# Kernel tuning notes

Measured on AMD Instinct MI355X. Metric: run time of the kernel, lower is better.

## Reference

```python
import jax, jax.numpy as jnp
import numpy as np

BSZ, SEQ, DIM, NH = 2, 2048, 2048, 16
HD = DIM // NH  # 128


def setup_inputs() -> dict:
    key = jax.random.key(0)
    ks = jax.random.split(key, 6)
    x = jax.random.normal(ks[0], (BSZ, SEQ, DIM), dtype=jnp.float32)
    # torch Linear weights: [out_features, in_features]
    scale = 1.0 / np.sqrt(DIM)
    wq = jax.random.normal(ks[1], (DIM, DIM), dtype=jnp.float32) * scale
    wk = jax.random.normal(ks[2], (DIM, DIM), dtype=jnp.float32) * scale
    wv = jax.random.normal(ks[3], (DIM, DIM), dtype=jnp.float32) * scale
    wo = jax.random.normal(ks[4], (DIM, DIM), dtype=jnp.float32) * scale
    # RoPE freqs (llama style): theta=10000
    inv_freq = 1.0 / (10000.0 ** (jnp.arange(0, HD, 2, dtype=jnp.float32) / HD))  # [HD//2]
    t = jnp.arange(SEQ, dtype=jnp.float32)
    angles = jnp.outer(t, inv_freq)  # [SEQ, HD//2]
    freqs_cos = jnp.cos(angles)
    freqs_sin = jnp.sin(angles)
    # causal additive mask [SEQ, SEQ]
    mask = jnp.where(jnp.tril(jnp.ones((SEQ, SEQ), dtype=bool)), 0.0, -jnp.inf).astype(jnp.float32)
    return {"x": x, "wq": wq, "wk": wk, "wv": wv, "wo": wo,
            "freqs_cos": freqs_cos, "freqs_sin": freqs_sin, "mask": mask}


def _apply_rope(v, cos, sin):
    # v: [b, s, h, hd]; complex pairs are interleaved (even=real, odd=imag)
    b, s, h, hd = v.shape
    vr = v.reshape(b, s, h, hd // 2, 2)
    v0, v1 = vr[..., 0], vr[..., 1]
    c = cos[None, :, None, :]  # [1, s, 1, hd//2]
    sn = sin[None, :, None, :]
    out = jnp.stack([v0 * c - v1 * sn, v0 * sn + v1 * c], axis=-1)
    return out.reshape(b, s, h, hd)


def reference(x, wq, wk, wv, wo, freqs_cos, freqs_sin, mask):
    b, s, _ = x.shape
    xq = (x @ wq.T).reshape(b, s, NH, HD)
    xk = (x @ wk.T).reshape(b, s, NH, HD)
    xv = (x @ wv.T).reshape(b, s, NH, HD)
    xq = _apply_rope(xq, freqs_cos, freqs_sin)
    xk = _apply_rope(xk, freqs_cos, freqs_sin)
    # [b, h, s, s]
    scores = jnp.einsum('bqhd,bkhd->bhqk', xq, xk) / jnp.sqrt(jnp.float32(HD))
    scores = scores + mask[None, None, :, :]
    probs = jax.nn.softmax(scores.astype(jnp.float32), axis=-1).astype(scores.dtype)
    out = jnp.einsum('bhqk,bkhd->bqhd', probs, xv).reshape(b, s, NH * HD)
    return out @ wo.T
```

## Files before the change

### kernel.cpp

```cpp
#include <hip/hip_runtime.h>
#include <hip/hip_bf16.h>
#include <stdint.h>

typedef __bf16 bf16x8 __attribute__((ext_vector_type(8)));
typedef float f32x4 __attribute__((ext_vector_type(4)));
typedef unsigned short u16;
typedef unsigned int u32;

#define DEVI __device__ __forceinline__

DEVI u16 f2b(float f){ __bf16 h = (__bf16)f; return __builtin_bit_cast(u16, h); }
DEVI float b2f(u16 u){ return (float)__builtin_bit_cast(__bf16, u); }

constexpr int BSZ = 2, SEQ = 2048, DIM = 2048, NH = 16, HD = 128;

#if defined(__has_builtin)
#if __has_builtin(__builtin_amdgcn_global_load_lds)
#define HAVE_ASYNC_LDS 1
#endif
#endif

DEVI void cp16(void* lds, const void* g){
#ifdef HAVE_ASYNC_LDS
  auto gp = (const __attribute__((address_space(1))) u32*)(uintptr_t)g;
  auto lp = (__attribute__((address_space(3))) u32*)(uintptr_t)lds;
  __builtin_amdgcn_global_load_lds(gp, lp, 16, 0, 0);
#else
  *(uint4*)lds = *(const uint4*)g;
#endif
}

__global__ __launch_bounds__(256) void k_convert(
    const float* __restrict__ x, const float* __restrict__ wq,
    const float* __restrict__ wk, const float* __restrict__ wv,
    const float* __restrict__ wo,
    u16* __restrict__ xb, u16* __restrict__ wqkv, u16* __restrict__ wob)
{
  int e = (blockIdx.x * 256 + threadIdx.x) * 4;
  float4 v; u16* dp;
  if (e < 8388608){
    v = *(const float4*)&x[e]; dp = &xb[e];
  } else if (e < 20971520){
    int o = e - 8388608; int sec = o >> 22; int oo = o & 4194303;
    const float* w = (sec == 0) ? wq : ((sec == 1) ? wk : wv);
    v = *(const float4*)&w[oo]; dp = &wqkv[o];
  } else {
    int o = e - 20971520;
    v = *(const float4*)&wo[o]; dp = &wob[o];
  }
  ushort4 r; r.x = f2b(v.x); r.y = f2b(v.y); r.z = f2b(v.z); r.w = f2b(v.w);
  *(ushort4*)dp = r;
}

DEVI void gemm_core_256x128(u16* smem, const u16* __restrict__ A, const u16* __restrict__ B,
                            int tm, int tn, int t, f32x4 (&acc)[4][4])
{
  const int lane = t & 63, l15 = lane & 15, quad = lane >> 4;
  const int wave = t >> 6, wm = wave >> 1, wn = wave & 1;
  const int swr = (l15 & 7) << 3;
  const int rb = t >> 3;
  const int csw = ((t & 7) ^ (rb & 7)) << 3;
  const u16* As0 = A + (size_t)(tm + rb) * DIM + csw;
  const u16* Bs0 = B + (size_t)(tn + rb) * DIM + csw;

  auto STAGE = [&](int kt){
    const int buf = kt & 1;
    const int kb = kt * 64;
    u16* d = &smem[buf * 24576 + t * 8];
    #pragma unroll
    for (int p = 0; p < 4; ++p)
      cp16(d + p * 4096, As0 + (size_t)p * (64 * DIM) + kb);
    #pragma unroll
    for (int p = 0; p < 2; ++p)
      cp16(d + 16384 + p * 4096, Bs0 + (size_t)p * (64 * DIM) + kb);
  };

  STAGE(0);
  #pragma unroll 2
  for (int kt = 0; kt < DIM / 64; ++kt){
    __syncthreads();
    if (kt < DIM / 64 - 1) STAGE(kt + 1);
    const u16* Ab = &smem[(kt & 1) * 24576];
    const u16* Bb = Ab + 16384;
    bf16x8 Af[4][2], Bf[4][2];
    #pragma unroll
    for (int mt = 0; mt < 4; ++mt)
      #pragma unroll
      for (int ks = 0; ks < 2; ++ks)
        Af[mt][ks] = *(const bf16x8*)&Ab[(wm * 64 + mt * 16 + l15) * 64 + ((ks * 32 + quad * 8) ^ swr)];
    #pragma unroll
    for (int nt = 0; nt < 4; ++nt)
      #pragma unroll
      for (int ks = 0; ks < 2; ++ks)
        Bf[nt][ks] = *(const bf16x8*)&Bb[(wn * 64 + nt * 16 + l15) * 64 + ((ks * 32 + quad * 8) ^ swr)];
    #pragma unroll
    for (int c = 0; c < 4; ++c){
      const int mb = (c >> 1) * 2, nb = (c & 1) * 2;
      __builtin_amdgcn_s_setprio(1);
      #pragma unroll
      for (int mi = 0; mi < 2; ++mi)
        #pragma unroll
        for (int ni = 0; ni < 2; ++ni)
          #pragma unroll
          for (int ks = 0; ks < 2; ++ks)
            acc[mb + mi][nb + ni] = __builtin_amdgcn_mfma_f32_16x16x32_bf16(
                Af[mb + mi][ks], Bf[nb + ni][ks], acc[mb + mi][nb + ni], 0, 0, 0);
      __builtin_amdgcn_s_setprio(0);
    }
  }
  __syncthreads();
}

__global__ __launch_bounds__(512, 2) void k_gemm_qkv(
    const u16* __restrict__ A, const u16* __restrict__ W,
    const float* __restrict__ fc, const float* __restrict__ fs,
    u16* __restrict__ Qd, u16* __restrict__ Kd, u16* __restrict__ Vd)
{
  __shared__ __align__(16) u16 smem[49152];
  const int t = threadIdx.x;
  const int wg = blockIdx.x;
  const int id = (wg & 7) * 96 + (wg >> 3);
  const int tm = (id & 15) << 8;
  const int tn = (id >> 4) << 7;
  f32x4 acc[4][4] = {};
  gemm_core_256x128(smem, A, W, tm, tn, t, acc);

  const int lane = t & 63, l15 = lane & 15, quad = lane >> 4;
  const int wave = t >> 6, wm = wave >> 1, wn = wave & 1;
  u16* Cs = smem;
  #pragma unroll
  for (int mt = 0; mt < 4; ++mt)
    #pragma unroll
    for (int nt = 0; nt < 4; ++nt)
      #pragma unroll
      for (int r = 0; r < 4; ++r){
        int rin = wm * 64 + mt * 16 + quad * 4 + r;
        int col = wn * 64 + nt * 16 + l15;
        Cs[rin * 128 + ((col + rin * 8) & 127)] = f2b(acc[mt][nt][r]);
      }
  __syncthreads();

  const int sec = tn >> 11;
  const int hh = (tn & 2047) >> 7;
  u16* dst = (sec == 0) ? Qd : ((sec == 1) ? Kd : Vd);
  const float qs = (sec == 0) ? (0.08838834764831845f * 1.4426950408889634f) : 1.0f;
  const int col0 = (t & 15) * 8;
  #pragma unroll
  for (int jj = 0; jj < 8; ++jj){
    int row = (t >> 4) + jj * 32;
    int m = tm + row;
    int b = m >> 11, s = m & 2047;
    uint4 cv = *(const uint4*)&Cs[row * 128 + ((col0 + row * 8) & 127)];
    const u16* cp = (const u16*)&cv;
    u16 op[8];
    if (sec < 2){
      float4 c4 = *(const float4*)&fc[(size_t)s * 64 + (col0 >> 1)];
      float4 s4 = *(const float4*)&fs[(size_t)s * 64 + (col0 >> 1)];
      float cc[4] = {c4.x*qs, c4.y*qs, c4.z*qs, c4.w*qs};
      float ss[4] = {s4.x*qs, s4.y*qs, s4.z*qs, s4.w*qs};
      #pragma unroll
      for (int p = 0; p < 4; ++p){
        float a = b2f(cp[2*p]), bb = b2f(cp[2*p+1]);
        op[2*p]   = f2b(a*cc[p] - bb*ss[p]);
        op[2*p+1] = f2b(a*ss[p] + bb*cc[p]);
      }
    } else {
      #pragma unroll
      for (int p = 0; p < 8; ++p) op[p] = cp[p];
    }
    *(uint4*)&dst[((size_t)(b*NH + hh)*SEQ + s)*HD + col0] = *(const uint4*)op;
  }
}

__global__ __launch_bounds__(256) void k_vtrans(
    const u16* __restrict__ V, u16* __restrict__ Vt)
{
  __shared__ u16 ts[64*72];
  const int t = threadIdx.x;
  const int st = blockIdx.x, dt = blockIdx.y, bh = blockIdx.z;
  const size_t base  = (size_t)bh * SEQ * HD;
  const size_t baseT = (size_t)bh * HD * SEQ;
  #pragma unroll
  for (int i = 0; i < 2; ++i){
    int s = i*32 + (t>>3), c = t&7;
    *(uint4*)&ts[s*72 + c*8] = *(const uint4*)&V[base + (size_t)(st*64 + s)*HD + dt*64 + c*8];
  }
  __syncthreads();
  #pragma unroll
  for (int i = 0; i < 2; ++i){
    int d = i*32 + (t>>3), sc = t&7;
    u16 tmp[8];
    #pragma unroll
    for (int j = 0; j < 8; ++j) tmp[j] = ts[(sc*8 + j)*72 + d];
    *(uint4*)&Vt[baseT + (size_t)(dt*64 + d)*SEQ + st*64 + sc*8] = *(const uint4*)tmp;
  }
}

__global__ __launch_bounds__(512) void k_flash(
    const u16* __restrict__ Qd, const u16* __restrict__ Kd,
    const u16* __restrict__ Vt, u16* __restrict__ OP0, u16* __restrict__ OP1,
    float* __restrict__ Mp, float* __restrict__ Lp)
{
  __shared__ __align__(16) u16 lds[24576];
  const int t = threadIdx.x, lane = t & 63, wave = t >> 6;
  const int l15 = lane & 15, quad = lane >> 4;
  const int swz = (l15 & 7) << 3;

  const int flat = blockIdx.x;
  const int xcd = flat & 7, idx = flat >> 3;
  const int bh = xcd * 4 + (idx >> 4);
  const int x = idx & 15;
  const int b = bh >> 4, h = bh & 15;
  const int j = x >> 1, split = x & 1;

  const size_t base  = (size_t)bh * SEQ * HD;
  const size_t baseT = (size_t)bh * HD * SEQ;
  u16* Ks = lds;
  u16* Vs = lds + 8192;
  u16* Psw = lds + 16384 + wave * 1024;
  u16* OPs = split ? OP1 : OP0;
  const int lo = 17*split, hi = lo + 17;
  const int qt0 = j, qt1 = 15 - j;
  const int len0 = 2*qt0 + 2;

  const int krow = t >> 4, kslot = t & 15;
  const int vrow = t >> 3, vslot = t & 7;

  for (int pass = 0; pass < 2; ++pass){
    const int qt = pass ? qt1 : qt0;
    const int len = 2*qt + 2;
    int kt0 = pass ? (lo - len0) : lo; if (kt0 < 0) kt0 = 0;
    int kt1 = pass ? (hi - len0) : hi; if (kt1 > len) kt1 = len;
    const int qb = qt*128 + wave*16;

    bf16x8 qf[4];
    #pragma unroll
    for (int ks = 0; ks < 4; ++ks)
      qf[ks] = *(const bf16x8*)&Qd[base + (size_t)(qb + l15)*HD + ks*32 + quad*8];

    f32x4 oacc[8] = {};
    float m_s = -1e30f, l_s = 0.f;

    if (kt0 < kt1){
      uint4 kreg[2], vreg[2];
      #pragma unroll
      for (int i = 0; i < 2; ++i){
        kreg[i] = *(const uint4*)&Kd[base + (size_t)(kt0*64 + i*32 + krow)*HD + kslot*8];
        vreg[i] = *(const uint4*)&Vt[baseT + (size_t)(i*64 + vrow)*SEQ + kt0*64 + vslot*8];
      }
      for (int kt = kt0; kt < kt1; ++kt){
        __syncthreads();
        #pragma unroll
        for (int i = 0; i < 2; ++i){
          int kr = i*32 + krow;
          *(uint4*)&Ks[kr*128 + ((kslot*8) ^ ((kr & 7) << 3))] = kreg[i];
          int vr = i*64 + vrow;
          *(uint4*)&Vs[vr*64 + ((vslot ^ (vr & 7)) << 3)] = vreg[i];
        }
        __syncthreads();
        if (kt + 1 < kt1){
          #pragma unroll
          for (int i = 0; i < 2; ++i){
            kreg[i] = *(const uint4*)&Kd[base + (size_t)((kt+1)*64 + i*32 + krow)*HD + kslot*8];
            vreg[i] = *(const uint4*)&Vt[baseT + (size_t)(i*64 + vrow)*SEQ + (kt+1)*64 + vslot*8];
          }
        }
        if (kt*64 <= qb + 15){
          f32x4 sacc[4] = {};
          #pragma unroll
          for (int ks = 0; ks < 4; ++ks){
            bf16x8 kf[4];
            #pragma unroll
            for (int nk = 0; nk < 4; ++nk)
              kf[nk] = *(const bf16x8*)&Ks[(nk*16 + l15)*128 + ((ks*32 + quad*8) ^ swz)];
            __builtin_amdgcn_s_setprio(1);
            #pragma unroll
            for (int nk = 0; nk < 4; ++nk)
              sacc[nk] = __builtin_amdgcn_mfma_f32_16x16x32_bf16(kf[nk], qf[ks], sacc[nk], 0, 0, 0);
            __builtin_amdgcn_s_setprio(0);
          }
          if (kt*64 + 63 > qb){
            int q = qb + l15;
            #pragma unroll
            for (int nk = 0; nk < 4; ++nk)
              #pragma unroll
              for (int r = 0; r < 4; ++r){
                int key = kt*64 + nk*16 + quad*4 + r;
                if (key > q) sacc[nk][r] = -1e30f;
              }
          }
          float m4[4];
          #pragma unroll
          for (int nk = 0; nk < 4; ++nk)
            m4[nk] = fmaxf(fmaxf(sacc[nk][0], sacc[nk][1]), fmaxf(sacc[nk][2], sacc[nk][3]));
          float rm = fmaxf(fmaxf(m4[0], m4[1]), fmaxf(m4[2], m4[3]));
          rm = fmaxf(rm, __shfl_xor(rm, 16));
          rm = fmaxf(rm, __shfl_xor(rm, 32));
          float mnew = fmaxf(m_s, rm);
          float alpha = exp2f(m_s - mnew);
          m_s = mnew;
          float s4[4];
          #pragma unroll
          for (int nk = 0; nk < 4; ++nk){
            u16 pk[4];
            float p0 = exp2f(sacc[nk][0] - mnew);
            float p1 = exp2f(sacc[nk][1] - mnew);
            float p2 = exp2f(sacc[nk][2] - mnew);
            float p3 = exp2f(sacc[nk][3] - mnew);
            pk[0] = f2b(p0); pk[1] = f2b(p1); pk[2] = f2b(p2); pk[3] = f2b(p3);
            s4[nk] = (p0 + p1) + (p2 + p3);
            *(uint2*)&Psw[l15*64 + ((nk*16 + quad*4) ^ swz)] = *(const uint2*)pk;
          }
          float rs = (s4[0] + s4[1]) + (s4[2] + s4[3]);
          rs += __shfl_xor(rs, 16);
          rs += __shfl_xor(rs, 32);
          l_s = l_s*alpha + rs;
          #pragma unroll
          for (int db = 0; db < 8; ++db)
            #pragma unroll
            for (int r = 0; r < 4; ++r) oacc[db][r] *= alpha;
          #pragma unroll
          for (int k2 = 0; k2 < 2; ++k2){
            bf16x8 pf = *(const bf16x8*)&Psw[l15*64 + ((k2*32 + quad*8) ^ swz)];
            __builtin_amdgcn_s_setprio(1);
            #pragma unroll
            for (int db = 0; db < 8; ++db){
              bf16x8 vf = *(const bf16x8*)&Vs[(db*16 + l15)*64 + ((k2*32 + quad*8) ^ swz)];
              oacc[db] = __builtin_amdgcn_mfma_f32_16x16x32_bf16(vf, pf, oacc[db], 0, 0, 0);
            }
            __builtin_amdgcn_s_setprio(0);
          }
        }
      }
    }
    __syncthreads();
    {
      u16* Osw = lds + wave*2048;
      #pragma unroll
      for (int db = 0; db < 8; ++db){
        u16 ok[4];
        #pragma unroll
        for (int r = 0; r < 4; ++r) ok[r] = f2b(oacc[db][r]);
        *(uint2*)&Osw[l15*128 + ((db*16 + quad*4) ^ swz)] = *(const uint2*)ok;
      }
      #pragma unroll
      for (int i = 0; i < 4; ++i){
        int q = i*4 + quad;
        uint4 v = *(const uint4*)&Osw[q*128 + ((l15*8) ^ ((q & 7) << 3))];
        *(uint4*)&OPs[(((size_t)(b*SEQ + qb + q))*NH + h)*HD + l15*8] = v;
      }
      if (quad == 0){
        size_t mi = ((size_t)split*BSZ*NH + bh)*SEQ + (qb + l15);
        Mp[mi] = m_s;
        Lp[mi] = l_s;
      }
    }
  }
}

__global__ __launch_bounds__(256) void k_combine(
    u16* __restrict__ OP0, const u16* __restrict__ OP1,
    const float* __restrict__ Mp, const float* __restrict__ Lp)
{
  size_t flat = ((size_t)blockIdx.x*256 + threadIdx.x)*8;
  int h = (int)((flat >> 7) & 15);
  int s = (int)((flat >> 11) & 2047);
  int b = (int)(flat >> 22);
  size_t row = ((size_t)(b*NH + h))*SEQ + s;
  const size_t off1 = (size_t)BSZ*NH*SEQ;
  float m0 = Mp[row], l0 = Lp[row];
  float m1 = Mp[row + off1], l1 = Lp[row + off1];
  float m = fmaxf(m0, m1);
  float w0 = exp2f(m0 - m), w1 = exp2f(m1 - m);
  float inv = 1.0f / (w0*l0 + w1*l1);
  uint4 a = *(const uint4*)&OP0[flat];
  uint4 c = *(const uint4*)&OP1[flat];
  const u16* pa = (const u16*)&a;
  const u16* pc = (const u16*)&c;
  u16 o[8];
  #pragma unroll
  for (int i = 0; i < 8; ++i)
    o[i] = f2b((b2f(pa[i])*w0 + b2f(pc[i])*w1) * inv);
  *(uint4*)&OP0[flat] = *(const uint4*)o;
}

__global__ __launch_bounds__(512, 2) void k_gemm_out(
    const u16* __restrict__ A, const u16* __restrict__ W, float* __restrict__ out)
{
  __shared__ __align__(16) u16 smem[49152];
  const int t = threadIdx.x;
  const int wg = blockIdx.x;
  const int id = (wg & 7) * 32 + (wg >> 3);
  const int tm = (id & 15) << 8;
  const int tn = (id >> 4) << 7;
  f32x4 acc[4][4] = {};
  gemm_core_256x128(smem, A, W, tm, tn, t, acc);
  const int lane = t & 63, l15 = lane & 15, quad = lane >> 4;
  const int wave = t >> 6, wm = wave >> 1, wn = wave & 1;
  #pragma unroll
  for (int mt = 0; mt < 4; ++mt)
    #pragma unroll
    for (int nt = 0; nt < 4; ++nt)
      #pragma unroll
      for (int r = 0; r < 4; ++r){
        int row = tm + wm*64 + mt*16 + quad*4 + r;
        int col = tn + wn*64 + nt*16 + l15;
        out[(size_t)row*DIM + col] = acc[mt][nt][r];
      }
}

extern "C" void kernel_launch(void* const* d_in, const int* in_sizes, int n_in,
                              void* d_out, int out_size, void* d_ws, size_t ws_size,
                              hipStream_t stream)
{
  const float* x  = (const float*)d_in[0];
  const float* wq = (const float*)d_in[1];
  const float* wk = (const float*)d_in[2];
  const float* wv = (const float*)d_in[3];
  const float* wo = (const float*)d_in[4];
  const float* fc = (const float*)d_in[5];
  const float* fs = (const float*)d_in[6];
  float* out = (float*)d_out;

  char* ws = (char*)d_ws;
  u16* xb   = (u16*)(ws);
  u16* wqkv = (u16*)(ws + 16777216);
  u16* wob  = (u16*)(ws + 41943040);
  u16* Qr   = (u16*)(ws + 50331648);
  u16* Kr   = (u16*)(ws + 67108864);
  u16* Vr   = (u16*)(ws + 83886080);
  u16* Ob   = (u16*)(ws + 100663296);
  u16* VtT  = xb;
  u16* OP1  = wqkv;
  float* Mp = (float*)(ws + 33554432);
  float* Lp = (float*)(ws + 34078720);

  k_convert <<<24576, 256, 0, stream>>>(x, wq, wk, wv, wo, xb, wqkv, wob);
  k_gemm_qkv<<<768, 512, 0, stream>>>(xb, wqkv, fc, fs, Qr, Kr, Vr);
  k_vtrans  <<<dim3(32, 2, 32), 256, 0, stream>>>(Vr, VtT);
  k_flash   <<<512, 512, 0, stream>>>(Qr, Kr, VtT, Ob, OP1, Mp, Lp);
  k_combine <<<4096, 256, 0, stream>>>(Ob, OP1, Mp, Lp);
  k_gemm_out<<<256, 512, 0, stream>>>(Ob, wob, out);
}
```

Baseline: 453.0 us.

## Load K/V fragments directly from global memory per wave, dropping LDS staging and barriers

Each wave now reads its K and V^T MFMA fragments straight from global memory instead of staging shared 64-key tiles in LDS behind block-wide barriers. Each wave also stops its key loop at its own causal limit, so waves no longer idle through tiles that other waves need. This removes the syncthreads and LDS store traffic but multiplies global/L2 reads by the number of waves and exposes load latency with no prefetch. The LDS layout is shrunk to only the P and O staging buffers.

```diff
diff --git a/kernel.cpp b/kernel.cpp
--- a/kernel.cpp
+++ b/kernel.cpp
@@ -215,16 +215,12 @@
 
   const size_t base  = (size_t)bh * SEQ * HD;
   const size_t baseT = (size_t)bh * HD * SEQ;
-  u16* Ks = lds;
-  u16* Vs = lds + 8192;
-  u16* Psw = lds + 16384 + wave * 1024;
+  u16* Psw = lds + wave * 1024;
+  u16* Osw = lds + 8192 + wave * 2048;
   u16* OPs = split ? OP1 : OP0;
   const int lo = 17*split, hi = lo + 17;
   const int qt0 = j, qt1 = 15 - j;
   const int len0 = 2*qt0 + 2;
-
-  const int krow = t >> 4, kslot = t & 15;
-  const int vrow = t >> 3, vslot = t & 7;
 
   for (int pass = 0; pass < 2; ++pass){
     const int qt = pass ? qt1 : qt0;
@@ -232,6 +228,7 @@
     int kt0 = pass ? (lo - len0) : lo; if (kt0 < 0) kt0 = 0;
     int kt1 = pass ? (hi - len0) : hi; if (kt1 > len) kt1 = len;
     const int qb = qt*128 + wave*16;
+    const int ktw = min(kt1, ((qb + 15) >> 6) + 1);
 
     bf16x8 qf[4];
     #pragma unroll
@@ -241,101 +238,75 @@
     f32x4 oacc[8] = {};
     float m_s = -1e30f, l_s = 0.f;
 
-    if (kt0 < kt1){
-      uint4 kreg[2], vreg[2];
-      #pragma unroll
-      for (int i = 0; i < 2; ++i){
-        kreg[i] = *(const uint4*)&Kd[base + (size_t)(kt0*64 + i*32 + krow)*HD + kslot*8];
-        vreg[i] = *(const uint4*)&Vt[baseT + (size_t)(i*64 + vrow)*SEQ + kt0*64 + vslot*8];
-      }
-      for (int kt = kt0; kt < kt1; ++kt){
-        __syncthreads();
-        #pragma unroll
-        for (int i = 0; i < 2; ++i){
-          int kr = i*32 + krow;
-          *(uint4*)&Ks[kr*128 + ((kslot*8) ^ ((kr & 7) << 3))] = kreg[i];
-          int vr = i*64 + vrow;
-          *(uint4*)&Vs[vr*64 + ((vslot ^ (vr & 7)) << 3)] = vreg[i];
-        }
-        __syncthreads();
-        if (kt + 1 < kt1){
+    for (int kt = kt0; kt < ktw; ++kt){
+      f32x4 sacc[4] = {};
+      #pragma unroll
+      for (int ks = 0; ks < 4; ++ks){
+        bf16x8 kf[4];
+        #pragma unroll
+        for (int nk = 0; nk < 4; ++nk)
+          kf[nk] = *(const bf16x8*)&Kd[base + (size_t)(kt*64 + nk*16 + l15)*HD + ks*32 + quad*8];
+        __builtin_amdgcn_s_setprio(1);
+        #pragma unroll
+        for (int nk = 0; nk < 4; ++nk)
+          sacc[nk] = __builtin_amdgcn_mfma_f32_16x16x32_bf16(kf[nk], qf[ks], sacc[nk], 0, 0, 0);
+        __builtin_amdgcn_s_setprio(0);
+      }
+      if (kt*64 + 63 > qb){
+        int q = qb + l15;
+        #pragma unroll
+        for (int nk = 0; nk < 4; ++nk)
           #pragma unroll
-          for (int i = 0; i < 2; ++i){
-            kreg[i] = *(const uint4*)&Kd[base + (size_t)((kt+1)*64 + i*32 + krow)*HD + kslot*8];
-            vreg[i] = *(const uint4*)&Vt[baseT + (size_t)(i*64 + vrow)*SEQ + (kt+1)*64 + vslot*8];
+          for (int r = 0; r < 4; ++r){
+            int key = kt*64 + nk*16 + quad*4 + r;
+            if (key > q) sacc[nk][r] = -1e30f;
           }
-        }
-        if (kt*64 <= qb + 15){
-          f32x4 sacc[4] = {};
-          #pragma unroll
-          for (int ks = 0; ks < 4; ++ks){
-            bf16x8 kf[4];
-            #pragma unroll
-            for (int nk = 0; nk < 4; ++nk)
-              kf[nk] = *(const bf16x8*)&Ks[(nk*16 + l15)*128 + ((ks*32 + quad*8) ^ swz)];
-            __builtin_amdgcn_s_setprio(1);
-            #pragma unroll
-            for (int nk = 0; nk < 4; ++nk)
-              sacc[nk] = __builtin_amdgcn_mfma_f32_16x16x32_bf16(kf[nk], qf[ks], sacc[nk], 0, 0, 0);
-            __builtin_amdgcn_s_setprio(0);
-          }
-          if (kt*64 + 63 > qb){
-            int q = qb + l15;
-            #pragma unroll
-            for (int nk = 0; nk < 4; ++nk)
-              #pragma unroll
-              for (int r = 0; r < 4; ++r){
-                int key = kt*64 + nk*16 + quad*4 + r;
-                if (key > q) sacc[nk][r] = -1e30f;
-              }
-          }
-          float m4[4];
-          #pragma unroll
-          for (int nk = 0; nk < 4; ++nk)
-            m4[nk] = fmaxf(fmaxf(sacc[nk][0], sacc[nk][1]), fmaxf(sacc[nk][2], sacc[nk][3]));
-          float rm = fmaxf(fmaxf(m4[0], m4[1]), fmaxf(m4[2], m4[3]));
-          rm = fmaxf(rm, __shfl_xor(rm, 16));
-          rm = fmaxf(rm, __shfl_xor(rm, 32));
-          float mnew = fmaxf(m_s, rm);
-          float alpha = exp2f(m_s - mnew);
-          m_s = mnew;
-          float s4[4];
-          #pragma unroll
-          for (int nk = 0; nk < 4; ++nk){
-            u16 pk[4];
-            float p0 = exp2f(sacc[nk][0] - mnew);
-            float p1 = exp2f(sacc[nk][1] - mnew);
-            float p2 = exp2f(sacc[nk][2] - mnew);
-            float p3 = exp2f(sacc[nk][3] - mnew);
-            pk[0] = f2b(p0); pk[1] = f2b(p1); pk[2] = f2b(p2); pk[3] = f2b(p3);
-            s4[nk] = (p0 + p1) + (p2 + p3);
-            *(uint2*)&Psw[l15*64 + ((nk*16 + quad*4) ^ swz)] = *(const uint2*)pk;
-          }
-          float rs = (s4[0] + s4[1]) + (s4[2] + s4[3]);
-          rs += __shfl_xor(rs, 16);
-          rs += __shfl_xor(rs, 32);
-          l_s = l_s*alpha + rs;
-          #pragma unroll
-          for (int db = 0; db < 8; ++db)
-            #pragma unroll
-            for (int r = 0; r < 4; ++r) oacc[db][r] *= alpha;
-          #pragma unroll
-          for (int k2 = 0; k2 < 2; ++k2){
-            bf16x8 pf = *(const bf16x8*)&Psw[l15*64 + ((k2*32 + quad*8) ^ swz)];
-            __builtin_amdgcn_s_setprio(1);
-            #pragma unroll
-            for (int db = 0; db < 8; ++db){
-              bf16x8 vf = *(const bf16x8*)&Vs[(db*16 + l15)*64 + ((k2*32 + quad*8) ^ swz)];
-              oacc[db] = __builtin_amdgcn_mfma_f32_16x16x32_bf16(vf, pf, oacc[db], 0, 0, 0);
-            }
-            __builtin_amdgcn_s_setprio(0);
-          }
-        }
+      }
+      float m4[4];
+      #pragma unroll
+      for (int nk = 0; nk < 4; ++nk)
+        m4[nk] = fmaxf(fmaxf(sacc[nk][0], sacc[nk][1]), fmaxf(sacc[nk][2], sacc[nk][3]));
+      float rm = fmaxf(fmaxf(m4[0], m4[1]), fmaxf(m4[2], m4[3]));
+      rm = fmaxf(rm, __shfl_xor(rm, 16));
+      rm = fmaxf(rm, __shfl_xor(rm, 32));
+      float mnew = fmaxf(m_s, rm);
+      float alpha = exp2f(m_s - mnew);
+      m_s = mnew;
+      float s4[4];
+      #pragma unroll
+      for (int nk = 0; nk < 4; ++nk){
+        u16 pk[4];
+        float p0 = exp2f(sacc[nk][0] - mnew);
+        float p1 = exp2f(sacc[nk][1] - mnew);
+        float p2 = exp2f(sacc[nk][2] - mnew);
+        float p3 = exp2f(sacc[nk][3] - mnew);
+        pk[0] = f2b(p0); pk[1] = f2b(p1); pk[2] = f2b(p2); pk[3] = f2b(p3);
+        s4[nk] = (p0 + p1) + (p2 + p3);
+        *(uint2*)&Psw[l15*64 + ((nk*16 + quad*4) ^ swz)] = *(const uint2*)pk;
+      }
+      float rs = (s4[0] + s4[1]) + (s4[2] + s4[3]);
+      rs += __shfl_xor(rs, 16);
+      rs += __shfl_xor(rs, 32);
+      l_s = l_s*alpha + rs;
+      #pragma unroll
+      for (int db = 0; db < 8; ++db)
+        #pragma unroll
+        for (int r = 0; r < 4; ++r) oacc[db][r] *= alpha;
+      #pragma unroll
+      for (int k2 = 0; k2 < 2; ++k2){
+        bf16x8 pf = *(const bf16x8*)&Psw[l15*64 + ((k2*32 + quad*8) ^ swz)];
+        bf16x8 vf[8];
+        #pragma unroll
+        for (int db = 0; db < 8; ++db)
+          vf[db] = *(const bf16x8*)&Vt[baseT + (size_t)(db*16 + l15)*SEQ + kt*64 + k2*32 + quad*8];
+        __builtin_amdgcn_s_setprio(1);
+        #pragma unroll
+        for (int db = 0; db < 8; ++db)
+          oacc[db] = __builtin_amdgcn_mfma_f32_16x16x32_bf16(vf[db], pf, oacc[db], 0, 0, 0);
+        __builtin_amdgcn_s_setprio(0);
       }
     }
-    __syncthreads();
     {
-      u16* Osw = lds + wave*2048;
       #pragma unroll
       for (int db = 0; db < 8; ++db){
         u16 ok[4];
```

After: 546.1 us. 1.21x slower.

## Double-buffer K/V tiles in LDS to halve barriers per key tile

Applied to the files above, without the earlier changes.

Allocates two LDS buffers for the K and V tiles so the next tile is written to the alternate buffer after computing on the current one, needing one barrier per iteration instead of two. The output epilogue now stages through each wave's private P scratch region in two 64-column chunks, so the barrier before the epilogue is dropped. LDS use grows from 48KB to 80KB per block, which may reduce occupancy for the 512-thread blocks.

```diff
diff --git a/kernel.cpp b/kernel.cpp
--- a/kernel.cpp
+++ b/kernel.cpp
@@ -201,7 +201,7 @@
     const u16* __restrict__ Vt, u16* __restrict__ OP0, u16* __restrict__ OP1,
     float* __restrict__ Mp, float* __restrict__ Lp)
 {
-  __shared__ __align__(16) u16 lds[24576];
+  __shared__ __align__(16) u16 lds[40960];
   const int t = threadIdx.x, lane = t & 63, wave = t >> 6;
   const int l15 = lane & 15, quad = lane >> 4;
   const int swz = (l15 & 7) << 3;
@@ -215,9 +215,7 @@
 
   const size_t base  = (size_t)bh * SEQ * HD;
   const size_t baseT = (size_t)bh * HD * SEQ;
-  u16* Ks = lds;
-  u16* Vs = lds + 8192;
-  u16* Psw = lds + 16384 + wave * 1024;
+  u16* Psw = lds + 32768 + wave * 1024;
   u16* OPs = split ? OP1 : OP0;
   const int lo = 17*split, hi = lo + 17;
   const int qt0 = j, qt1 = 15 - j;
@@ -243,36 +241,40 @@
 
     if (kt0 < kt1){
       uint4 kreg[2], vreg[2];
-      #pragma unroll
-      for (int i = 0; i < 2; ++i){
-        kreg[i] = *(const uint4*)&Kd[base + (size_t)(kt0*64 + i*32 + krow)*HD + kslot*8];
-        vreg[i] = *(const uint4*)&Vt[baseT + (size_t)(i*64 + vrow)*SEQ + kt0*64 + vslot*8];
-      }
-      for (int kt = kt0; kt < kt1; ++kt){
-        __syncthreads();
+      auto LOADT = [&](int kt){
+        #pragma unroll
+        for (int i = 0; i < 2; ++i){
+          kreg[i] = *(const uint4*)&Kd[base + (size_t)(kt*64 + i*32 + krow)*HD + kslot*8];
+          vreg[i] = *(const uint4*)&Vt[baseT + (size_t)(i*64 + vrow)*SEQ + kt*64 + vslot*8];
+        }
+      };
+      auto WRITET = [&](int bu){
+        u16* Kb = lds + bu*8192;
+        u16* Vb = lds + 16384 + bu*8192;
         #pragma unroll
         for (int i = 0; i < 2; ++i){
           int kr = i*32 + krow;
-          *(uint4*)&Ks[kr*128 + ((kslot*8) ^ ((kr & 7) << 3))] = kreg[i];
+          *(uint4*)&Kb[kr*128 + ((kslot*8) ^ ((kr & 7) << 3))] = kreg[i];
           int vr = i*64 + vrow;
-          *(uint4*)&Vs[vr*64 + ((vslot ^ (vr & 7)) << 3)] = vreg[i];
-        }
-        __syncthreads();
-        if (kt + 1 < kt1){
-          #pragma unroll
-          for (int i = 0; i < 2; ++i){
-            kreg[i] = *(const uint4*)&Kd[base + (size_t)((kt+1)*64 + i*32 + krow)*HD + kslot*8];
-            vreg[i] = *(const uint4*)&Vt[baseT + (size_t)(i*64 + vrow)*SEQ + (kt+1)*64 + vslot*8];
-          }
-        }
+          *(uint4*)&Vb[vr*64 + ((vslot*8) ^ ((vr & 7) << 3))] = vreg[i];
+        }
+      };
+      LOADT(kt0);
+      WRITET(0);
+      if (kt0 + 1 < kt1) LOADT(kt0 + 1);
+      __syncthreads();
+      int buf = 0;
+      for (int kt = kt0; kt < kt1; ++kt){
         if (kt*64 <= qb + 15){
+          const u16* Kb = lds + buf*8192;
+          const u16* Vb = lds + 16384 + buf*8192;
           f32x4 sacc[4] = {};
           #pragma unroll
           for (int ks = 0; ks < 4; ++ks){
             bf16x8 kf[4];
             #pragma unroll
             for (int nk = 0; nk < 4; ++nk)
-              kf[nk] = *(const bf16x8*)&Ks[(nk*16 + l15)*128 + ((ks*32 + quad*8) ^ swz)];
+              kf[nk] = *(const bf16x8*)&Kb[(nk*16 + l15)*128 + ((ks*32 + quad*8) ^ swz)];
             __builtin_amdgcn_s_setprio(1);
             #pragma unroll
             for (int nk = 0; nk < 4; ++nk)
@@ -325,29 +327,39 @@
             __builtin_amdgcn_s_setprio(1);
             #pragma unroll
             for (int db = 0; db < 8; ++db){
-              bf16x8 vf = *(const bf16x8*)&Vs[(db*16 + l15)*64 + ((k2*32 + quad*8) ^ swz)];
+              bf16x8 vf = *(const bf16x8*)&Vb[(db*16 + l15)*64 + ((k2*32 + quad*8) ^ swz)];
               oacc[db] = __builtin_amdgcn_mfma_f32_16x16x32_bf16(vf, pf, oacc[db], 0, 0, 0);
             }
             __builtin_amdgcn_s_setprio(0);
           }
         }
+        if (kt + 1 < kt1){
+          WRITET(buf ^ 1);
+          if (kt + 2 < kt1) LOADT(kt + 2);
+          __syncthreads();
+        }
+        buf ^= 1;
       }
     }
-    __syncthreads();
     {
-      u16* Osw = lds + wave*2048;
-      #pragma unroll
-      for (int db = 0; db < 8; ++db){
-        u16 ok[4];
+      u16* Ow = Psw;
+      const int qrow = lane >> 2;
+      #pragma unroll
+      for (int ch = 0; ch < 2; ++ch){
         #pragma unroll
-        for (int r = 0; r < 4; ++r) ok[r] = f2b(oacc[db][r]);
-        *(uint2*)&Osw[l15*128 + ((db*16 + quad*4) ^ swz)] = *(const uint2*)ok;
-      }
-      #pragma unroll
-      for (int i = 0; i < 4; ++i){
-        int q = i*4 + quad;
-        uint4 v = *(const uint4*)&Osw[q*128 + ((l15*8) ^ ((q & 7) << 3))];
-        *(uint4*)&OPs[(((size_t)(b*SEQ + qb + q))*NH + h)*HD + l15*8] = v;
+        for (int db2 = 0; db2 < 4; ++db2){
+          int db = ch*4 + db2;
+          u16 ok[4];
+          #pragma unroll
+          for (int r = 0; r < 4; ++r) ok[r] = f2b(oacc[db][r]);
+          *(uint2*)&Ow[l15*64 + ((db2*16 + quad*4) ^ swz)] = *(const uint2*)ok;
+        }
+        #pragma unroll
+        for (int i = 0; i < 2; ++i){
+          int c8 = (lane & 3) + i*4;
+          uint4 v = *(const uint4*)&Ow[qrow*64 + ((c8*8) ^ ((qrow & 7) << 3))];
+          *(uint4*)&OPs[(((size_t)(b*SEQ + qb + qrow))*NH + h)*HD + ch*64 + c8*8] = v;
+        }
       }
       if (quad == 0){
         size_t mi = ((size_t)split*BSZ*NH + bh)*SEQ + (qb + l15);
@@ -355,6 +367,7 @@
         Lp[mi] = l_s;
       }
     }
+    __syncthreads();
   }
 }
 
```

New measurement: 439.7 us. -2.9%, faster.
